# Kernel optimization log

Hardware: AMD Instinct MI355X
Metric: run time of the kernel (lower is better)

Reference implementation:

```python
import jax, jax.numpy as jnp
import numpy as np
from jax import lax

# ---- module constants (mirror CorrelatedSphericalField.__init__) ----
NLAT = 361
NLON = 2 * NLAT
LMAX = NLAT            # number of degrees l
MMAX = NLAT + 1        # number of orders m = nlon//2 + 1
N_LATENT = 16
T_STEPS = 8
LENGTH_SCALE = 500_000.0
TIME_SCALE = 48.0
SIGMA = 0.3
DT = 6.0
R_EARTH = 6_371_000.0
PHI = float(np.exp(-DT / TIME_SCALE))
KT = (LENGTH_SCALE / R_EARTH) ** 2 / 2.0
FOUR_PI = float(4.0 * np.pi)


def _precompute_pct():
    """Associated Legendre tensor pct[m, l, k] for InverseRealSHT,
    equiangular grid, norm='backward' (orthonormal P / sqrt(4pi)), with
    Condon-Shortley phase -- matches torch_harmonics _precompute_legpoly(inverse=True)."""
    theta = np.linspace(0.0, np.pi, NLAT)      # equiangular incl. poles
    x = np.cos(theta)
    s = np.sin(theta)
    nmax = max(MMAX, LMAX)
    vdm = np.zeros((nmax, nmax, NLAT), dtype=np.float64)  # [m, l, lat]
    vdm[0, 0] = 1.0 / np.sqrt(4.0 * np.pi)
    for m in range(1, nmax):                    # diagonal P_m^m
        vdm[m, m] = np.sqrt((2.0 * m + 1.0) / (2.0 * m)) * s * vdm[m - 1, m - 1]
    for m in range(nmax - 1):                   # P_{m+1}^m
        vdm[m, m + 1] = np.sqrt(2.0 * m + 3.0) * x * vdm[m, m]
    for l in range(2, nmax):                    # three-term recurrence, vectorized over m
        ms = np.arange(l - 1)
        a = np.sqrt((4.0 * l * l - 1.0) / (l * l - ms * ms))[:, None]
        b = np.sqrt(((l - 1.0) ** 2 - ms * ms) / (4.0 * (l - 1.0) ** 2 - 1.0))[:, None]
        vdm[ms, l] = a * (x[None, :] * vdm[ms, l - 1] - b * vdm[ms, l - 2])
    vdm[1::2] *= -1.0                           # Condon-Shortley phase
    pct = vdm[:MMAX, :LMAX] / np.sqrt(4.0 * np.pi)  # norm='backward', inverse=True
    return jnp.asarray(pct, dtype=jnp.float32)


def _make_sigma_n():
    j = np.arange(1, NLAT, dtype=np.float64)
    denom = 2.0 * np.sum((2.0 * j + 1.0) * np.exp(-KT * j * (j + 1.0)))
    F0 = np.sqrt(SIGMA ** 2 * (1.0 - PHI ** 2) / denom)
    l = np.arange(NLAT, dtype=np.float64)
    prods = np.repeat((l * (l + 1.0))[:, None], MMAX, axis=1)   # (nlat, nlat+1)
    sn = np.tril(np.exp(-KT * prods / 2.0) * F0)                # keep m <= l
    return jnp.asarray(sn, dtype=jnp.float32)


def setup_inputs() -> dict:
    key = jax.random.key(0)
    k0, k1 = jax.random.split(key)
    sigma_n = _make_sigma_n()
    # initial stationary AR(1) coefficients: (1-phi^2)^{-1/2} * sigma_n * xi0
    xi0 = jax.random.normal(k0, (N_LATENT, LMAX, MMAX, 2), dtype=jnp.float32)
    coeff0 = (1.0 - PHI ** 2) ** (-0.5) * sigma_n[None, :, :, None] * xi0
    # pre-drawn innovations for the T AR(1) updates (real/imag stacked)
    xi = jax.random.normal(k1, (T_STEPS, N_LATENT, LMAX, MMAX, 2), dtype=jnp.float32)
    pct = _precompute_pct()
    x = jnp.zeros((T_STEPS,), dtype=jnp.int32)   # only x.shape[0] is used
    return {"x": x, "sigma_n": sigma_n, "coeff0": coeff0, "xi": xi, "pct": pct}


def reference(x, sigma_n, coeff0, xi, pct):
    T = x.shape[0]
    c0 = coeff0[..., 0] + 1j * coeff0[..., 1]    # (N, L, M) complex64
    xic = xi[..., 0] + 1j * xi[..., 1]           # (T, N, L, M) complex64

    # AR(1): emit coeff BEFORE update (matches the torch loop ordering)
    def step(c, xk):
        return PHI * c + sigma_n * xk, c

    _, coeffs = lax.scan(step, c0, xic[:T])      # (T, N, L, M)

    # inverse real SHT, batched over all T steps at once:
    # xs[..., k, m] = sum_l coeff[..., l, m] * pct[m, l, k]
    re = jnp.einsum('tnlm,mlk->tnkm', coeffs.real, pct)
    im = jnp.einsum('tnlm,mlk->tnkm', coeffs.imag, pct)
    xs = re + 1j * im                            # (T, N, nlat, mmax)
    out = jnp.fft.irfft(xs, n=NLON, axis=-1, norm='forward') * FOUR_PI
    return out.reshape(T, 1, 1, N_LATENT, NLAT, NLON)
```

## Files before the change

kernel.cpp:

```cpp
#include <hip/hip_runtime.h>
#include <math.h>

#define NLATC   361
#define NLONC   722
#define MMAXC   362
#define LMAXC   361
#define NLK     16
#define TSTEPS  8
#define LCUT    128
#define MCUT    128
#define MCK     256
#define TNK     46208
#define NPAD    768
#define KPAD    384
#define PHI_F   0.8824969025845955f
#define FOURPI  12.566370614359172f
#define ASCALE  1024.0f
#define OSCALE  0.0009765625f

typedef _Float16 half8 __attribute__((ext_vector_type(8)));
typedef float floatx4 __attribute__((ext_vector_type(4)));

#define GLOAD16(g, l) __builtin_amdgcn_global_load_lds( \
    (const __attribute__((address_space(1))) void*)(g), \
    (__attribute__((address_space(3))) void*)(l), 16, 0, 0)

__global__ __launch_bounds__(256) void k_prep(const float* __restrict__ sigma_n,
                                              const float* __restrict__ coeff0,
                                              const float* __restrict__ xi,
                                              const float* __restrict__ pct,
                                              _Float16* __restrict__ Bf,
                                              _Float16* __restrict__ pTf,
                                              _Float16* __restrict__ cB) {
    __shared__ _Float16 sm[64][66];
    int bid = blockIdx.x;
    int tid = threadIdx.x;

    if (bid < 768) {
        int idx = bid * 256 + tid;
        int j = idx >> 8, mc = idx & 255;
        int m = mc >> 1, c = mc & 1;
        float v = 0.0f;
        if (j < NLONC) {
            int r = (m * j) % NLONC;
            float th = (float)r * (6.283185307179586f / 722.0f);
            float s, co;
            sincosf(th, &s, &co);
            float wq = (m == 0 ? 1.0f : 2.0f) * FOURPI;
            v = c ? (-wq * s) : (wq * co);
        }
        Bf[idx] = (_Float16)v;
    } else if (bid < 2304) {
        int b = bid - 768;
        int k0 = (b % 6) * 64;
        int l0 = ((b / 6) & 1) * 64;
        int m  = b / 12;
        int tx = tid & 63, ty = tid >> 6;
#pragma unroll
        for (int i = 0; i < 16; ++i) {
            int row = ty * 16 + i;
            int k = k0 + tx;
            sm[row][tx] = (k < NLATC)
                ? (_Float16)pct[((size_t)m * LMAXC + l0 + row) * NLATC + k] : (_Float16)0.0f;
        }
        __syncthreads();
#pragma unroll
        for (int i = 0; i < 16; ++i) {
            int kr = ty * 16 + i;
            pTf[((size_t)m * KPAD + k0 + kr) * 128 + l0 + tx] = sm[tx][kr];
        }
    } else {
        int b = bid - 2304;
        int mt = b & 3, lt = (b >> 2) & 1, n = b >> 3;
        int ml = tid & 31, lg = tid >> 5;
        int m  = mt * 32 + ml;
        int l0 = lt * 64 + lg * 8;
        float cr[8], ci[8], sg[8];
#pragma unroll
        for (int i = 0; i < 8; ++i) {
            int l = l0 + i;
            sg[i] = sigma_n[(size_t)l * MMAXC + m];
            float2 c0 = *(const float2*)&coeff0[(((size_t)n * LMAXC + l) * MMAXC + m) * 2];
            cr[i] = c0.x; ci[i] = c0.y;
        }
#pragma unroll
        for (int t = 0; t < TSTEPS; ++t) {
            half8 hr, hi;
#pragma unroll
            for (int i = 0; i < 8; ++i) {
                hr[i] = (_Float16)(cr[i] * ASCALE);
                hi[i] = (_Float16)(ci[i] * ASCALE);
            }
            size_t rowR = ((size_t)m * 256 +       t * 16 + n) * 128 + l0;
            size_t rowI = ((size_t)m * 256 + 128 + t * 16 + n) * 128 + l0;
            *(half8*)&cB[rowR] = hr;
            *(half8*)&cB[rowI] = hi;
            if (t < TSTEPS - 1) {
#pragma unroll
                for (int i = 0; i < 8; ++i) {
                    float2 x = *(const float2*)
                        &xi[((((size_t)t * NLK + n) * LMAXC + l0 + i) * MMAXC + m) * 2];
                    cr[i] = PHI_F * cr[i] + sg[i] * x.x;
                    ci[i] = PHI_F * ci[i] + sg[i] * x.y;
                }
            }
        }
    }
}

__global__ __launch_bounds__(256) void k_leg(const _Float16* __restrict__ cB,
                                             const _Float16* __restrict__ pTf,
                                             _Float16* __restrict__ xsTh) {
    __shared__ _Float16 As[256][32];
    __shared__ _Float16 Bs[64][32];
    int tid = threadIdx.x;
    int k0c = blockIdx.x * 64;
    int m   = blockIdx.y;
    int w = tid >> 6, lane = tid & 63, m16 = lane & 15, quad = lane >> 4;
    int rA = lane >> 2;
    int cA = (lane & 3) * 8;
    floatx4 acc[4][4];
#pragma unroll
    for (int i = 0; i < 4; ++i)
#pragma unroll
        for (int j = 0; j < 4; ++j) acc[i][j] = (floatx4)(0.0f);

    int lt0 = m & ~31;
    for (int lt = lt0; lt < 128; lt += 32) {
#pragma unroll
        for (int c = 0; c < 4; ++c) {
            int rr = w * 64 + c * 16;
            GLOAD16(&cB[((size_t)m * 256 + rr + rA) * 128 + lt + cA], &As[rr][0]);
        }
        {
            int rr = w * 16;
            GLOAD16(&pTf[((size_t)m * KPAD + k0c + rr + rA) * 128 + lt + cA], &Bs[rr][0]);
        }
        __syncthreads();
        half8 a[4], b[4];
#pragma unroll
        for (int i = 0; i < 4; ++i) a[i] = *(const half8*)&As[w * 64 + i * 16 + m16][quad * 8];
#pragma unroll
        for (int j = 0; j < 4; ++j) b[j] = *(const half8*)&Bs[j * 16 + m16][quad * 8];
#pragma unroll
        for (int i = 0; i < 4; ++i)
#pragma unroll
            for (int j = 0; j < 4; ++j)
                acc[i][j] = __builtin_amdgcn_mfma_f32_16x16x32_f16(a[i], b[j], acc[i][j], 0, 0, 0);
        __syncthreads();
    }
#pragma unroll
    for (int i = 0; i < 4; ++i)
#pragma unroll
        for (int j = 0; j < 4; ++j)
#pragma unroll
            for (int reg = 0; reg < 4; ++reg) {
                int r = w * 64 + i * 16 + quad * 4 + reg;
                int c = r >> 7, tn = r & 127;
                int k = k0c + j * 16 + m16;
                if (k < NLATC)
                    xsTh[(size_t)(2 * m + c) * TNK + tn * NLATC + k] = (_Float16)acc[i][j][reg];
            }
}

__global__ __launch_bounds__(256) void k_castXs(const _Float16* __restrict__ xsTh,
                                                _Float16* __restrict__ xsA) {
    __shared__ _Float16 sm[64][66];
    int tx = threadIdx.x & 63, ty = threadIdx.x >> 6;
    int t0  = blockIdx.x * 64;
    int mc0 = blockIdx.y * 64;
#pragma unroll
    for (int i = 0; i < 16; ++i) {
        int row = ty * 16 + i;
        sm[row][tx] = xsTh[(size_t)(mc0 + row) * TNK + t0 + tx];
    }
    __syncthreads();
#pragma unroll
    for (int i = 0; i < 16; ++i) {
        int row = ty * 16 + i;
        xsA[(size_t)(t0 + row) * MCK + mc0 + tx] = sm[tx][row];
    }
}

__global__ __launch_bounds__(256) void k_gemm2(const _Float16* __restrict__ A,
                                               const _Float16* __restrict__ Bf,
                                               float* __restrict__ C) {
    __shared__ _Float16 As[128][32];
    __shared__ _Float16 Bs[128][32];
    int tid = threadIdx.x;
    int w = tid >> 6, lane = tid & 63, m16 = lane & 15, quad = lane >> 4;
    int lin = blockIdx.y * 6 + blockIdx.x;
    int xcd = lin & 7, idx = lin >> 3;
    int wg  = (xcd < 6) ? xcd * 271 + idx : 1626 + (xcd - 6) * 270 + idx;
    int row0 = (wg / 6) * 128;
    int j0   = (wg % 6) * 128;
    int wr = (w & 1) * 64, wc = (w >> 1) * 64;
    int rA = lane >> 2, cA = (lane & 3) * 8;
    floatx4 acc[4][4];
#pragma unroll
    for (int i = 0; i < 4; ++i)
#pragma unroll
        for (int j = 0; j < 4; ++j) acc[i][j] = (floatx4)(0.0f);

    for (int k0 = 0; k0 < MCK; k0 += 32) {
#pragma unroll
        for (int c = 0; c < 2; ++c) {
            int rr = w * 32 + c * 16;
            GLOAD16(&A [(size_t)(row0 + rr + rA) * MCK + k0 + cA], &As[rr][0]);
            GLOAD16(&Bf[(size_t)(j0   + rr + rA) * MCK + k0 + cA], &Bs[rr][0]);
        }
        __syncthreads();
        half8 a[4], b[4];
#pragma unroll
        for (int i = 0; i < 4; ++i) a[i] = *(const half8*)&As[wr + i * 16 + m16][quad * 8];
#pragma unroll
        for (int j = 0; j < 4; ++j) b[j] = *(const half8*)&Bs[wc + j * 16 + m16][quad * 8];
#pragma unroll
        for (int i = 0; i < 4; ++i)
#pragma unroll
            for (int j = 0; j < 4; ++j)
                acc[i][j] = __builtin_amdgcn_mfma_f32_16x16x32_f16(a[i], b[j], acc[i][j], 0, 0, 0);
        __syncthreads();
    }
#pragma unroll
    for (int i = 0; i < 4; ++i)
#pragma unroll
        for (int j = 0; j < 4; ++j)
#pragma unroll
            for (int reg = 0; reg < 4; ++reg) {
                int row = row0 + wr + i * 16 + quad * 4 + reg;
                int col = j0 + wc + j * 16 + m16;
                if (col < NLONC)
                    C[(size_t)row * NLONC + col] = acc[i][j][reg] * OSCALE;
            }
}

extern "C" void kernel_launch(void* const* d_in, const int* in_sizes, int n_in,
                              void* d_out, int out_size, void* d_ws, size_t ws_size,
                              hipStream_t stream) {
    (void)in_sizes; (void)n_in; (void)out_size; (void)ws_size;
    const float* sigma_n = (const float*)d_in[1];
    const float* coeff0  = (const float*)d_in[2];
    const float* xi      = (const float*)d_in[3];
    const float* pct     = (const float*)d_in[4];
    float* out = (float*)d_out;

    char* ws = (char*)d_ws;
    size_t off = 0;
    _Float16* cB   = (_Float16*)(ws + off); off += (size_t)128 * 256 * 128 * 2;
    _Float16* pTf  = (_Float16*)(ws + off); off += (size_t)128 * KPAD * 128 * 2;
    _Float16* xsTh = (_Float16*)(ws + off); off += (size_t)MCK * TNK * 2;
    _Float16* xsA  = (_Float16*)(ws + off); off += (size_t)TNK * MCK * 2;
    _Float16* Bf   = (_Float16*)(ws + off); off += (size_t)NPAD * MCK * 2;

    k_prep<<<2432, 256, 0, stream>>>(sigma_n, coeff0, xi, pct, Bf, pTf, cB);
    k_leg<<<dim3(6, 128), 256, 0, stream>>>(cB, pTf, xsTh);
    k_castXs<<<dim3(722, 4), 256, 0, stream>>>(xsTh, xsA);
    k_gemm2<<<dim3(6, 361), 256, 0, stream>>>(xsA, Bf, out);
}
```

Baseline: 389.7 us.

## Fuse xs transpose into gemm2 A-tile load and drop castXs kernel

Removes the separate k_castXs transpose kernel and its workspace buffer. gemm2 now reads xsTh directly in its original (mc, tn*k) layout, transposes into a padded LDS tile through per-element stores, and register-prefetches the next k-slice. The coefficient-prep thread mapping is also changed to make m the slow index, which alters access coalescing. This saves one launch and a roughly 24 MB read/write round trip, at the cost of scattered 2-byte LDS stores and extra gemm2 work.

```diff
diff --git a/kernel.cpp b/kernel.cpp
--- a/kernel.cpp
+++ b/kernel.cpp
@@ -72,7 +72,7 @@
     } else {
         int b = bid - 2304;
         int mt = b & 3, lt = (b >> 2) & 1, n = b >> 3;
-        int ml = tid & 31, lg = tid >> 5;
+        int ml = tid >> 3, lg = tid & 7;
         int m  = mt * 32 + ml;
         int l0 = lt * 64 + lg * 8;
         float cr[8], ci[8], sg[8];
@@ -163,29 +163,10 @@
             }
 }
 
-__global__ __launch_bounds__(256) void k_castXs(const _Float16* __restrict__ xsTh,
-                                                _Float16* __restrict__ xsA) {
-    __shared__ _Float16 sm[64][66];
-    int tx = threadIdx.x & 63, ty = threadIdx.x >> 6;
-    int t0  = blockIdx.x * 64;
-    int mc0 = blockIdx.y * 64;
-#pragma unroll
-    for (int i = 0; i < 16; ++i) {
-        int row = ty * 16 + i;
-        sm[row][tx] = xsTh[(size_t)(mc0 + row) * TNK + t0 + tx];
-    }
-    __syncthreads();
-#pragma unroll
-    for (int i = 0; i < 16; ++i) {
-        int row = ty * 16 + i;
-        xsA[(size_t)(t0 + row) * MCK + mc0 + tx] = sm[tx][row];
-    }
-}
-
-__global__ __launch_bounds__(256) void k_gemm2(const _Float16* __restrict__ A,
+__global__ __launch_bounds__(256) void k_gemm2(const _Float16* __restrict__ xsTh,
                                                const _Float16* __restrict__ Bf,
                                                float* __restrict__ C) {
-    __shared__ _Float16 As[128][32];
+    __shared__ _Float16 As[128][40];
     __shared__ _Float16 Bs[128][32];
     int tid = threadIdx.x;
     int w = tid >> 6, lane = tid & 63, m16 = lane & 15, quad = lane >> 4;
@@ -195,21 +176,35 @@
     int row0 = (wg / 6) * 128;
     int j0   = (wg % 6) * 128;
     int wr = (w & 1) * 64, wc = (w >> 1) * 64;
-    int rA = lane >> 2, cA = (lane & 3) * 8;
+    int rB = lane >> 2, cb4 = (lane & 3) * 8;
+    int amc = tid >> 3, ach = tid & 7;
+    const _Float16* aSrc = &xsTh[(size_t)amc * TNK + row0 + ach * 16];
     floatx4 acc[4][4];
 #pragma unroll
     for (int i = 0; i < 4; ++i)
 #pragma unroll
         for (int j = 0; j < 4; ++j) acc[i][j] = (floatx4)(0.0f);
 
+    half8 pa0 = *(const half8*)(aSrc);
+    half8 pa1 = *(const half8*)(aSrc + 8);
+
+#pragma unroll
     for (int k0 = 0; k0 < MCK; k0 += 32) {
 #pragma unroll
         for (int c = 0; c < 2; ++c) {
             int rr = w * 32 + c * 16;
-            GLOAD16(&A [(size_t)(row0 + rr + rA) * MCK + k0 + cA], &As[rr][0]);
-            GLOAD16(&Bf[(size_t)(j0   + rr + rA) * MCK + k0 + cA], &Bs[rr][0]);
-        }
-        __syncthreads();
+            GLOAD16(&Bf[(size_t)(j0 + rr + rB) * MCK + k0 + cb4], &Bs[rr][0]);
+        }
+#pragma unroll
+        for (int e = 0; e < 8; ++e) As[ach * 16 + e][amc] = pa0[e];
+#pragma unroll
+        for (int e = 0; e < 8; ++e) As[ach * 16 + 8 + e][amc] = pa1[e];
+        __syncthreads();
+        if (k0 + 32 < MCK) {
+            const _Float16* p = aSrc + (size_t)(k0 + 32) * TNK;
+            pa0 = *(const half8*)(p);
+            pa1 = *(const half8*)(p + 8);
+        }
         half8 a[4], b[4];
 #pragma unroll
         for (int i = 0; i < 4; ++i) a[i] = *(const half8*)&As[wr + i * 16 + m16][quad * 8];
@@ -250,11 +245,9 @@
     _Float16* cB   = (_Float16*)(ws + off); off += (size_t)128 * 256 * 128 * 2;
     _Float16* pTf  = (_Float16*)(ws + off); off += (size_t)128 * KPAD * 128 * 2;
     _Float16* xsTh = (_Float16*)(ws + off); off += (size_t)MCK * TNK * 2;
-    _Float16* xsA  = (_Float16*)(ws + off); off += (size_t)TNK * MCK * 2;
     _Float16* Bf   = (_Float16*)(ws + off); off += (size_t)NPAD * MCK * 2;
 
     k_prep<<<2432, 256, 0, stream>>>(sigma_n, coeff0, xi, pct, Bf, pTf, cB);
     k_leg<<<dim3(6, 128), 256, 0, stream>>>(cB, pTf, xsTh);
-    k_castXs<<<dim3(722, 4), 256, 0, stream>>>(xsTh, xsA);
-    k_gemm2<<<dim3(6, 361), 256, 0, stream>>>(xsA, Bf, out);
-}
+    k_gemm2<<<dim3(6, 361), 256, 0, stream>>>(xsTh, Bf, out);
+}
```

Result: no change. 388.4 us (-0.3%).
